# Kernel tuning notes

Hardware: AMD Instinct MI355X
Metric: run time of the kernel (lower is better)

The kernel has to match this reference:

```python
import jax, jax.numpy as jnp
import numpy as np

V = 50257       # vocab size (leaves of Huffman tree)
N_DEC = V - 1   # internal decision nodes
D = 1024        # input_size
N_EX = 8192     # number of examples (tokens)
MAX_LEN = 24    # max Huffman path depth


def setup_inputs() -> dict:
    key = jax.random.key(0)
    k_x, k_w, k_t, k_p, k_c, k_l = jax.random.split(key, 6)
    x = jax.random.normal(k_x, (N_EX, D), dtype=jnp.float32)
    W = jax.random.normal(k_w, (N_DEC, D), dtype=jnp.float32) * 0.02
    t = jax.random.randint(k_t, (N_EX,), 0, V, dtype=jnp.int32)
    # padded per-leaf tree paths: decision-node indices and +/-1 branch codes
    paths = jax.random.randint(k_p, (V, MAX_LEN), 0, N_DEC, dtype=jnp.int32)
    codes = jnp.where(jax.random.bernoulli(k_c, 0.5, (V, MAX_LEN)), 1.0, -1.0).astype(jnp.float32)
    lens = jax.random.randint(k_l, (V,), 1, MAX_LEN + 1, dtype=jnp.int32)
    return {"x": x, "W": W, "t": t, "paths": paths, "codes": codes, "lens": lens}


def reference(x, W, t, paths, codes, lens):
    # Per-example tree path: gather the decision nodes / codes for each target leaf.
    node_idx = paths[t]            # [N_EX, MAX_LEN] int32
    code = codes[t]                # [N_EX, MAX_LEN] +/-1
    mask = (jnp.arange(MAX_LEN)[None, :] < lens[t][:, None]).astype(x.dtype)  # [N_EX, MAX_LEN]
    # Irregular gather of W rows along each path, then per-step dot products.
    Wp = W[node_idx]               # [N_EX, MAX_LEN, D]
    wxy = code * jnp.einsum('nd,nld->nl', x, Wp)   # [N_EX, MAX_LEN]
    # Per-decision binary log-loss: log(1 + exp(-wxy)), masked to true path length.
    ls = jax.nn.softplus(-wxy) * mask
    return ls.sum()
```

## Files before the change

### kernel.cpp

```cpp
#include <hip/hip_runtime.h>
#include <math.h>

#define HS_D       1024
#define HS_MAXLEN  24

__global__ __launch_bounds__(256) void hsm_loss_kernel(
    const float* __restrict__ x,
    const float* __restrict__ W,
    const int*   __restrict__ t,
    const int*   __restrict__ paths,
    const float* __restrict__ codes,
    const int*   __restrict__ lens,
    float*       __restrict__ out)
{
    const int n    = blockIdx.x;
    const int tid  = threadIdx.x;
    const int wave = tid >> 6;
    const int lane = tid & 63;

    const int leaf = t[n];
    const int L    = lens[leaf];

    const float4* x4 = (const float4*)(x + (size_t)n * HS_D);
    float4 xf[4];
#pragma unroll
    for (int j = 0; j < 4; ++j)
        xf[j] = x4[j * 64 + lane];

    float local = 0.0f;

    for (int l = wave; l < L; l += 4) {
        const int   node = paths[leaf * HS_MAXLEN + l];
        const float c    = codes[leaf * HS_MAXLEN + l];

        const float4* w4 = (const float4*)(W + (size_t)node * HS_D);
        float dot = 0.0f;
#pragma unroll
        for (int j = 0; j < 4; ++j) {
            const float4 wf = w4[j * 64 + lane];
            dot += xf[j].x * wf.x + xf[j].y * wf.y
                 + xf[j].z * wf.z + xf[j].w * wf.w;
        }

#pragma unroll
        for (int off = 32; off > 0; off >>= 1)
            dot += __shfl_down(dot, off);

        if (lane == 0) {
            const float z = -c * dot;
            local += fmaxf(z, 0.0f) + log1pf(expf(-fabsf(z)));
        }
    }

    __shared__ float s[4];
    if (lane == 0) s[wave] = local;
    __syncthreads();
    if (tid == 0) {
        const float blocksum = s[0] + s[1] + s[2] + s[3];
        atomicAdd(out, blocksum);
    }
}

extern "C" void kernel_launch(void* const* d_in, const int* in_sizes, int n_in,
                              void* d_out, int out_size, void* d_ws, size_t ws_size,
                              hipStream_t stream) {
    const float* x     = (const float*)d_in[0];
    const float* W     = (const float*)d_in[1];
    const int*   t     = (const int*)  d_in[2];
    const int*   paths = (const int*)  d_in[3];
    const float* codes = (const float*)d_in[4];
    const int*   lens  = (const int*)  d_in[5];
    float* out = (float*)d_out;

    const int n_ex = in_sizes[2];

    hipMemsetAsync(out, 0, sizeof(float), stream);

    hsm_loss_kernel<<<n_ex, 256, 0, stream>>>(x, W, t, paths, codes, lens, out);
}
```

Before: 362.4 us.

## Split path steps into per-wave pairs with bucketed atomics and finish kernel

Each wave now handles two consecutive path steps of one example rather than one block looping over all steps. This exposes more independent waves, issues both W-row loads up front for memory-level parallelism, and balances the uneven path lengths. Partial losses go through atomics into 512 workspace buckets to reduce contention, and a small second kernel reduces them. In exchange, x is reloaded once per wave instead of once per example, there is an extra kernel launch and memset, and waves whose steps fall beyond the path length exit early.

```diff
diff --git a/kernel.cpp b/kernel.cpp
--- a/kernel.cpp
+++ b/kernel.cpp
@@ -3,62 +3,87 @@
 
 #define HS_D       1024
 #define HS_MAXLEN  24
+#define HS_PAIRS   12
+#define HS_NBUCKET 512
 
-__global__ __launch_bounds__(256) void hsm_loss_kernel(
+__global__ __launch_bounds__(256) void hsm_pair_kernel(
     const float* __restrict__ x,
     const float* __restrict__ W,
     const int*   __restrict__ t,
     const int*   __restrict__ paths,
     const float* __restrict__ codes,
     const int*   __restrict__ lens,
-    float*       __restrict__ out)
+    float*       __restrict__ ws,
+    int n_ex)
 {
-    const int n    = blockIdx.x;
     const int tid  = threadIdx.x;
-    const int wave = tid >> 6;
     const int lane = tid & 63;
+    const int gw   = blockIdx.x * 4 + (tid >> 6);
+    const int n    = gw / HS_PAIRS;
+    const int p    = gw % HS_PAIRS;
 
     const int leaf = t[n];
     const int L    = lens[leaf];
+    const int l0   = 2 * p;
+    const int l1   = l0 + 1;
+    if (l0 >= L) return;
 
-    const float4* x4 = (const float4*)(x + (size_t)n * HS_D);
-    float4 xf[4];
+    const int   node0 = paths[leaf * HS_MAXLEN + l0];
+    const float c0    = codes[leaf * HS_MAXLEN + l0];
+    const bool  v1    = (l1 < L);
+    const int   node1 = v1 ? paths[leaf * HS_MAXLEN + l1] : node0;
+    const float c1    = v1 ? codes[leaf * HS_MAXLEN + l1] : 1.0f;
+
+    const float4* x4 = (const float4*)(x + (size_t)n     * HS_D);
+    const float4* w0 = (const float4*)(W + (size_t)node0 * HS_D);
+    const float4* w1 = (const float4*)(W + (size_t)node1 * HS_D);
+
+    float4 xf[4], wf0[4], wf1[4];
 #pragma unroll
-    for (int j = 0; j < 4; ++j)
-        xf[j] = x4[j * 64 + lane];
+    for (int j = 0; j < 4; ++j) xf[j]  = x4[j * 64 + lane];
+#pragma unroll
+    for (int j = 0; j < 4; ++j) wf0[j] = w0[j * 64 + lane];
+#pragma unroll
+    for (int j = 0; j < 4; ++j) wf1[j] = w1[j * 64 + lane];
 
-    float local = 0.0f;
-
-    for (int l = wave; l < L; l += 4) {
-        const int   node = paths[leaf * HS_MAXLEN + l];
-        const float c    = codes[leaf * HS_MAXLEN + l];
-
-        const float4* w4 = (const float4*)(W + (size_t)node * HS_D);
-        float dot = 0.0f;
+    float d0 = 0.0f, d1 = 0.0f;
 #pragma unroll
-        for (int j = 0; j < 4; ++j) {
-            const float4 wf = w4[j * 64 + lane];
-            dot += xf[j].x * wf.x + xf[j].y * wf.y
-                 + xf[j].z * wf.z + xf[j].w * wf.w;
-        }
+    for (int j = 0; j < 4; ++j) {
+        d0 += xf[j].x * wf0[j].x + xf[j].y * wf0[j].y
+            + xf[j].z * wf0[j].z + xf[j].w * wf0[j].w;
+        d1 += xf[j].x * wf1[j].x + xf[j].y * wf1[j].y
+            + xf[j].z * wf1[j].z + xf[j].w * wf1[j].w;
+    }
 
 #pragma unroll
-        for (int off = 32; off > 0; off >>= 1)
-            dot += __shfl_down(dot, off);
-
-        if (lane == 0) {
-            const float z = -c * dot;
-            local += fmaxf(z, 0.0f) + log1pf(expf(-fabsf(z)));
-        }
+    for (int off = 32; off > 0; off >>= 1) {
+        d0 += __shfl_down(d0, off);
+        d1 += __shfl_down(d1, off);
     }
 
-    __shared__ float s[4];
-    if (lane == 0) s[wave] = local;
-    __syncthreads();
-    if (tid == 0) {
-        const float blocksum = s[0] + s[1] + s[2] + s[3];
-        atomicAdd(out, blocksum);
+    if (lane == 0) {
+        const float z0 = -c0 * d0;
+        float v = fmaxf(z0, 0.0f) + log1pf(expf(-fabsf(z0)));
+        if (v1) {
+            const float z1 = -c1 * d1;
+            v += fmaxf(z1, 0.0f) + log1pf(expf(-fabsf(z1)));
+        }
+        atomicAdd(&ws[gw & (HS_NBUCKET - 1)], v);
     }
+}
+
+__global__ __launch_bounds__(64) void hsm_finish_kernel(
+    const float* __restrict__ ws, float* __restrict__ out)
+{
+    const int lane = threadIdx.x;
+    float s = 0.0f;
+#pragma unroll
+    for (int k = 0; k < HS_NBUCKET / 64; ++k)
+        s += ws[lane + 64 * k];
+#pragma unroll
+    for (int off = 32; off > 0; off >>= 1)
+        s += __shfl_down(s, off);
+    if (lane == 0) out[0] = s;
 }
 
 extern "C" void kernel_launch(void* const* d_in, const int* in_sizes, int n_in,
@@ -71,10 +96,15 @@
     const float* codes = (const float*)d_in[4];
     const int*   lens  = (const int*)  d_in[5];
     float* out = (float*)d_out;
+    float* ws  = (float*)d_ws;
 
     const int n_ex = in_sizes[2];
 
-    hipMemsetAsync(out, 0, sizeof(float), stream);
+    hipMemsetAsync(ws, 0, HS_NBUCKET * sizeof(float), stream);
 
-    hsm_loss_kernel<<<n_ex, 256, 0, stream>>>(x, W, t, paths, codes, lens, out);
+    const int n_waves  = n_ex * HS_PAIRS;
+    const int n_blocks = (n_waves + 3) / 4;
+    hsm_pair_kernel<<<n_blocks, 256, 0, stream>>>(x, W, t, paths, codes, lens,
+                                                  ws, n_ex);
+    hsm_finish_kernel<<<1, 64, 0, stream>>>(ws, out);
 }
```

Result: faster. 324.2 us (-10.5%).
